# Kernel tuning notes

Hardware: AMD Instinct MI355X
Metric: run time of the kernel (lower is better)

Reference implementation:

```python
import jax, jax.numpy as jnp
import numpy as np
import math

B, S, KV_DIM, Q_DIM, E, H = 16, 8192, 512, 512, 512, 8
D = E // H  # head_dim = 64


def setup_inputs() -> dict:
    key = jax.random.key(0)
    ks = jax.random.split(key, 12)
    s_q = 1.0 / math.sqrt(Q_DIM)
    s_kv = 1.0 / math.sqrt(KV_DIM)
    s_e = 1.0 / math.sqrt(E)
    return {
        "query": jax.random.normal(ks[0], (B, Q_DIM), dtype=jnp.float32),
        "key_value": jax.random.normal(ks[1], (B, S, KV_DIM), dtype=jnp.float32),
        "Wq": jax.random.uniform(ks[2], (Q_DIM, E), jnp.float32, -s_q, s_q),
        "bq": jax.random.uniform(ks[3], (E,), jnp.float32, -s_q, s_q),
        "Wk": jax.random.uniform(ks[4], (KV_DIM, E), jnp.float32, -s_kv, s_kv),
        "bk": jax.random.uniform(ks[5], (E,), jnp.float32, -s_kv, s_kv),
        "Wv": jax.random.uniform(ks[6], (KV_DIM, E), jnp.float32, -s_kv, s_kv),
        "bv": jax.random.uniform(ks[7], (E,), jnp.float32, -s_kv, s_kv),
        "Wo": jax.random.uniform(ks[8], (E, E), jnp.float32, -s_e, s_e),
        "bo": jax.random.uniform(ks[9], (E,), jnp.float32, -s_e, s_e),
    }


def reference(query, key_value, Wq, bq, Wk, bk, Wv, bv, Wo, bo):
    bsz, seq_len, _ = key_value.shape
    # q: [B, H, D] (single query per batch)
    q = (query @ Wq + bq).reshape(bsz, H, D)
    # k, v: [B, S, H, D]
    k = (key_value @ Wk + bk).reshape(bsz, seq_len, H, D)
    v = (key_value @ Wv + bv).reshape(bsz, seq_len, H, D)
    scale = 1.0 / math.sqrt(D)
    # attn logits: [B, H, S]
    attn = jnp.einsum("bhd,bshd->bhs", q, k) * scale
    weights = jax.nn.softmax(attn, axis=-1)
    # context: [B, H, D] -> [B, E]
    context = jnp.einsum("bhs,bshd->bhd", weights, v).reshape(bsz, E)
    return context @ Wo + bo
```

## Files before the change

kernel.cpp:

```cpp
#include <hip/hip_runtime.h>
#include <math.h>

#define B_   16
#define S_   8192
#define KVD  512
#define E_   512
#define H_   8
#define D_   64

#define OFF_QKVEC   0
#define OFF_QBUF    65536
#define OFF_LACC    73728
#define OFF_CTXACC  73856
#define OFF_CTXBUF  139392
#define WS_FLOATS   147584
#define ZERO_START  OFF_QBUF
#define ZERO_COUNT  82048

__global__ __launch_bounds__(256) void k_init(float* __restrict__ wsf,
                                              float* __restrict__ out) {
    int i = blockIdx.x * 256 + threadIdx.x;
    const int nws4 = ZERO_COUNT / 4;
    if (i < nws4) {
        *(float4*)&wsf[ZERO_START + i * 4] = make_float4(0.f, 0.f, 0.f, 0.f);
    } else if (i < nws4 + (B_ * E_) / 4) {
        *(float4*)&out[(i - nws4) * 4] = make_float4(0.f, 0.f, 0.f, 0.f);
    }
}

__global__ __launch_bounds__(512) void k_q(const float* __restrict__ query,
                                           const float* __restrict__ Wq,
                                           float* __restrict__ q_buf) {
    const int kc = blockIdx.x, b = blockIdx.y;
    const int e = threadIdx.x;
    __shared__ float qs[128];
    if (e < 128) qs[e] = query[(size_t)b * 512 + kc * 128 + e];
    __syncthreads();
    const float* wq = Wq + (size_t)(kc * 128) * E_ + e;
    float a0 = 0.f, a1 = 0.f, a2 = 0.f, a3 = 0.f;
    for (int k = 0; k < 128; k += 4) {
        a0 = fmaf(qs[k],     wq[(size_t)(k)     * E_], a0);
        a1 = fmaf(qs[k + 1], wq[(size_t)(k + 1) * E_], a1);
        a2 = fmaf(qs[k + 2], wq[(size_t)(k + 2) * E_], a2);
        a3 = fmaf(qs[k + 3], wq[(size_t)(k + 3) * E_], a3);
    }
    atomicAdd(&q_buf[(size_t)b * E_ + e], (a0 + a1) + (a2 + a3));
}

__global__ __launch_bounds__(256) void k_fold(const float* __restrict__ q_buf,
                                              const float* __restrict__ bq,
                                              const float* __restrict__ Wk,
                                              float* __restrict__ qk_vec) {
    const int cc = blockIdx.x, h = blockIdx.y;
    const int tid = threadIdx.x;
    const int c0 = cc * 64;
    __shared__ float wk[64 * 65];
    __shared__ float qh[16 * 64];

    #pragma unroll
    for (int k = 0; k < 4; ++k) {
        int f4i = tid + k * 256;
        int row = f4i >> 4, d4 = f4i & 15;
        float4 v = *(const float4*)&Wk[(size_t)(c0 + row) * E_ + h * D_ + d4 * 4];
        wk[row * 65 + d4 * 4 + 0] = v.x;
        wk[row * 65 + d4 * 4 + 1] = v.y;
        wk[row * 65 + d4 * 4 + 2] = v.z;
        wk[row * 65 + d4 * 4 + 3] = v.w;
    }
    #pragma unroll
    for (int k = 0; k < 4; ++k) {
        int idx = tid + k * 256;
        int b = idx >> 6, d = idx & 63;
        qh[idx] = (q_buf[(size_t)b * E_ + h * D_ + d] + bq[h * D_ + d]) * 0.125f;
    }
    __syncthreads();

    const int c_local = tid & 63, w = tid >> 6;
    float acc[4] = {0.f, 0.f, 0.f, 0.f};
    for (int d = 0; d < 64; ++d) {
        float wv = wk[c_local * 65 + d];
        #pragma unroll
        for (int i = 0; i < 4; ++i)
            acc[i] = fmaf(qh[(w * 4 + i) * 64 + d], wv, acc[i]);
    }
    #pragma unroll
    for (int i = 0; i < 4; ++i) {
        int b = w * 4 + i;
        qk_vec[((size_t)b * H_ + h) * KVD + c0 + c_local] = acc[i];
    }
}

#define SROW 68
#define RB   4

template <int NC>
__device__ __forceinline__ void attn_loadrows(float (&kvr)[RB][8],
                                              const float* __restrict__ base,
                                              int it, int lane) {
    #pragma unroll
    for (int r = 0; r < RB; ++r) {
        const float* rowp = base + (size_t)(it * RB + r) * KVD;
        float4 v0 = *(const float4*)&rowp[lane * 4];
        float4 v1 = *(const float4*)&rowp[256 + lane * 4];
        kvr[r][0] = v0.x; kvr[r][1] = v0.y; kvr[r][2] = v0.z; kvr[r][3] = v0.w;
        kvr[r][4] = v1.x; kvr[r][5] = v1.y; kvr[r][6] = v1.z; kvr[r][7] = v1.w;
    }
}

__device__ __forceinline__ void attn_process(const float (&kvr)[RB][8],
                                             const float (&qk)[H_][8],
                                             float (&ctx)[H_][8], float& l_run,
                                             float* __restrict__ wscr,
                                             const float* __restrict__ rdb,
                                             int lane) {
    const int seg = lane & 7;
    #pragma unroll
    for (int r = 0; r < RB; ++r)
        #pragma unroll
        for (int h = 0; h < H_; ++h) {
            float p = 0.f;
            #pragma unroll
            for (int j = 0; j < 8; ++j) p = fmaf(kvr[r][j], qk[h][j], p);
            wscr[(r * H_ + h) * SROW + lane] = p;
        }
    float e4[RB];
    #pragma unroll
    for (int r = 0; r < RB; ++r) {
        const float* p = rdb + r * H_ * SROW;
        float4 x = *(const float4*)p;
        float4 y = *(const float4*)(p + 4);
        float s = ((x.x + x.y) + (x.z + x.w)) + ((y.x + y.y) + (y.z + y.w));
        s += __shfl_xor(s, 1);
        s += __shfl_xor(s, 2);
        s += __shfl_xor(s, 4);
        e4[r] = __expf(s);
        l_run += e4[r];
    }
    #pragma unroll
    for (int r = 0; r < RB; ++r)
        #pragma unroll
        for (int h = 0; h < H_; ++h) {
            float wv = __shfl(e4[r], h * 8 + seg);
            #pragma unroll
            for (int j = 0; j < 8; ++j)
                ctx[h][j] = fmaf(wv, kvr[r][j], ctx[h][j]);
        }
}

template <int NC>
__global__ __launch_bounds__(256, 2) void k_attn(const float* __restrict__ kv,
                                                 const float* __restrict__ qk_vec,
                                                 float* __restrict__ ctx_acc,
                                                 float* __restrict__ l_acc) {
    constexpr int CHUNK = S_ / NC;
    constexpr int RPW = CHUNK / 4;
    constexpr int NIT = RPW / RB;
    constexpr int SPW = RB * H_ * SROW;

    __shared__ __align__(16) float scr[4 * SPW];
    __shared__ float lbuf[32];

    const int tid = threadIdx.x;
    const int lane = tid & 63;
    const int w = tid >> 6;
    const int nc = blockIdx.x, b = blockIdx.y;
    const int hme = lane >> 3, seg = lane & 7;

    float qk[H_][8];
    {
        const float* qb = qk_vec + (size_t)b * H_ * KVD;
        #pragma unroll
        for (int h = 0; h < H_; ++h) {
            float4 v0 = *(const float4*)&qb[h * KVD + lane * 4];
            float4 v1 = *(const float4*)&qb[h * KVD + 256 + lane * 4];
            qk[h][0] = v0.x; qk[h][1] = v0.y; qk[h][2] = v0.z; qk[h][3] = v0.w;
            qk[h][4] = v1.x; qk[h][5] = v1.y; qk[h][6] = v1.z; qk[h][7] = v1.w;
        }
    }

    float ctx[H_][8];
    #pragma unroll
    for (int h = 0; h < H_; ++h)
        #pragma unroll
        for (int j = 0; j < 8; ++j) ctx[h][j] = 0.f;
    float l_run = 0.f;

    float* wscr = scr + w * SPW;
    const float* rdb = wscr + hme * SROW + seg * 8;
    const float* kvbase = kv + ((size_t)b * S_ + (size_t)nc * CHUNK + (size_t)w * RPW) * KVD;

    float kvA[RB][8], kvB[RB][8];
    attn_loadrows<NC>(kvA, kvbase, 0, lane);
    #pragma unroll 1
    for (int it = 0; it < NIT; it += 2) {
        attn_loadrows<NC>(kvB, kvbase, it + 1, lane);
        attn_process(kvA, qk, ctx, l_run, wscr, rdb, lane);
        if (it + 2 < NIT) attn_loadrows<NC>(kvA, kvbase, it + 2, lane);
        attn_process(kvB, qk, ctx, l_run, wscr, rdb, lane);
    }

    if (seg == 0) lbuf[w * 8 + hme] = l_run;
    __syncthreads();
    float* cbuf = scr;
    if (w == 0) {
        #pragma unroll
        for (int h = 0; h < H_; ++h) {
            *(float4*)&cbuf[h * KVD + lane * 4] =
                make_float4(ctx[h][0], ctx[h][1], ctx[h][2], ctx[h][3]);
            *(float4*)&cbuf[h * KVD + 256 + lane * 4] =
                make_float4(ctx[h][4], ctx[h][5], ctx[h][6], ctx[h][7]);
        }
    }
    __syncthreads();
    if (w != 0) {
        #pragma unroll
        for (int h = 0; h < H_; ++h) {
            #pragma unroll
            for (int j = 0; j < 4; ++j)
                atomicAdd(&cbuf[h * KVD + lane * 4 + j], ctx[h][j]);
            #pragma unroll
            for (int j = 4; j < 8; ++j)
                atomicAdd(&cbuf[h * KVD + 256 + lane * 4 + (j - 4)], ctx[h][j]);
        }
    }
    __syncthreads();
    size_t gbase = (size_t)b * (H_ * KVD);
    #pragma unroll
    for (int k = 0; k < 16; ++k)
        atomicAdd(&ctx_acc[gbase + k * 256 + tid], cbuf[k * 256 + tid]);
    if (tid < H_) {
        float L = lbuf[tid] + lbuf[8 + tid] + lbuf[16 + tid] + lbuf[24 + tid];
        atomicAdd(&l_acc[b * H_ + tid], L);
    }
}

__global__ __launch_bounds__(512) void k_ctx(const float* __restrict__ ctx_acc,
                                             const float* __restrict__ l_acc,
                                             const float* __restrict__ Wv,
                                             const float* __restrict__ bv,
                                             float* __restrict__ ctx_buf) {
    const int kc = blockIdx.x, b = blockIdx.y;
    const int e = threadIdx.x;
    const int h = e >> 6;
    const float inv = 1.0f / l_acc[b * H_ + h];
    const float* ca = ctx_acc + ((size_t)b * H_ + h) * KVD + kc * 128;
    const float* wv = Wv + (size_t)(kc * 128) * E_ + e;
    float a0 = 0.f, a1 = 0.f, a2 = 0.f, a3 = 0.f;
    for (int c = 0; c < 128; c += 4) {
        a0 = fmaf(ca[c],     wv[(size_t)(c)     * E_], a0);
        a1 = fmaf(ca[c + 1], wv[(size_t)(c + 1) * E_], a1);
        a2 = fmaf(ca[c + 2], wv[(size_t)(c + 2) * E_], a2);
        a3 = fmaf(ca[c + 3], wv[(size_t)(c + 3) * E_], a3);
    }
    float val = ((a0 + a1) + (a2 + a3)) * inv;
    if (kc == 0) val += bv[e];
    atomicAdd(&ctx_buf[(size_t)b * E_ + e], val);
}

__global__ __launch_bounds__(512) void k_o(const float* __restrict__ ctx_buf,
                                           const float* __restrict__ Wo,
                                           const float* __restrict__ bo,
                                           float* __restrict__ out) {
    const int kc = blockIdx.x, b = blockIdx.y;
    const int e = threadIdx.x;
    const float* cs = ctx_buf + (size_t)b * E_ + kc * 128;
    const float* wo = Wo + (size_t)(kc * 128) * E_ + e;
    float a0 = 0.f, a1 = 0.f, a2 = 0.f, a3 = 0.f;
    for (int k = 0; k < 128; k += 4) {
        a0 = fmaf(cs[k],     wo[(size_t)(k)     * E_], a0);
        a1 = fmaf(cs[k + 1], wo[(size_t)(k + 1) * E_], a1);
        a2 = fmaf(cs[k + 2], wo[(size_t)(k + 2) * E_], a2);
        a3 = fmaf(cs[k + 3], wo[(size_t)(k + 3) * E_], a3);
    }
    float val = (a0 + a1) + (a2 + a3);
    if (kc == 0) val += bo[e];
    atomicAdd(&out[(size_t)b * E_ + e], val);
}

extern "C" void kernel_launch(void* const* d_in, const int* in_sizes, int n_in,
                              void* d_out, int out_size, void* d_ws, size_t ws_size,
                              hipStream_t stream) {
    const float* query = (const float*)d_in[0];
    const float* kv    = (const float*)d_in[1];
    const float* Wq    = (const float*)d_in[2];
    const float* bq    = (const float*)d_in[3];
    const float* Wk    = (const float*)d_in[4];
    const float* Wv    = (const float*)d_in[6];
    const float* bv    = (const float*)d_in[7];
    const float* Wo    = (const float*)d_in[8];
    const float* bo    = (const float*)d_in[9];
    float* out = (float*)d_out;
    float* wsf = (float*)d_ws;

    float* qk_vec  = wsf + OFF_QKVEC;
    float* q_buf   = wsf + OFF_QBUF;
    float* l_acc   = wsf + OFF_LACC;
    float* ctx_acc = wsf + OFF_CTXACC;
    float* ctx_buf = wsf + OFF_CTXBUF;

    constexpr int NC = 32;

    k_init<<<89, 256, 0, stream>>>(wsf, out);
    k_q<<<dim3(4, B_), 512, 0, stream>>>(query, Wq, q_buf);
    k_fold<<<dim3(8, H_), 256, 0, stream>>>(q_buf, bq, Wk, qk_vec);
    k_attn<NC><<<dim3(NC, B_), 256, 0, stream>>>(kv, qk_vec, ctx_acc, l_acc);
    k_ctx<<<dim3(4, B_), 512, 0, stream>>>(ctx_acc, l_acc, Wv, bv, ctx_buf);
    k_o<<<dim3(4, B_), 512, 0, stream>>>(ctx_buf, Wo, bo, out);
}
```

Measured before the change: 488.2 us.

## Fuse init, Q projection and K-fold into one prep kernel; relax attn launch bounds

Merges the zero-init, query projection and Wk fold kernels into a single k_prep launch. Each fold block now recomputes its head slice of the Q projection from the full query held in shared memory, which removes the q_buf atomics and two launches but adds redundant Wq reads across the 8 column blocks per head. It also changes k_attn launch bounds from 2 to 1 blocks per CU. That lets the compiler use more registers but may reduce occupancy.

Measured after the change: 454.4 us. 6.9% less time.

```diff
diff --git a/kernel.cpp b/kernel.cpp
--- a/kernel.cpp
+++ b/kernel.cpp
@@ -9,91 +9,96 @@
 #define D_   64
 
 #define OFF_QKVEC   0
-#define OFF_QBUF    65536
-#define OFF_LACC    73728
-#define OFF_CTXACC  73856
-#define OFF_CTXBUF  139392
-#define WS_FLOATS   147584
-#define ZERO_START  OFF_QBUF
-#define ZERO_COUNT  82048
-
-__global__ __launch_bounds__(256) void k_init(float* __restrict__ wsf,
-                                              float* __restrict__ out) {
-    int i = blockIdx.x * 256 + threadIdx.x;
-    const int nws4 = ZERO_COUNT / 4;
-    if (i < nws4) {
-        *(float4*)&wsf[ZERO_START + i * 4] = make_float4(0.f, 0.f, 0.f, 0.f);
-    } else if (i < nws4 + (B_ * E_) / 4) {
-        *(float4*)&out[(i - nws4) * 4] = make_float4(0.f, 0.f, 0.f, 0.f);
-    }
-}
-
-__global__ __launch_bounds__(512) void k_q(const float* __restrict__ query,
-                                           const float* __restrict__ Wq,
-                                           float* __restrict__ q_buf) {
-    const int kc = blockIdx.x, b = blockIdx.y;
-    const int e = threadIdx.x;
-    __shared__ float qs[128];
-    if (e < 128) qs[e] = query[(size_t)b * 512 + kc * 128 + e];
-    __syncthreads();
-    const float* wq = Wq + (size_t)(kc * 128) * E_ + e;
-    float a0 = 0.f, a1 = 0.f, a2 = 0.f, a3 = 0.f;
-    for (int k = 0; k < 128; k += 4) {
-        a0 = fmaf(qs[k],     wq[(size_t)(k)     * E_], a0);
-        a1 = fmaf(qs[k + 1], wq[(size_t)(k + 1) * E_], a1);
-        a2 = fmaf(qs[k + 2], wq[(size_t)(k + 2) * E_], a2);
-        a3 = fmaf(qs[k + 3], wq[(size_t)(k + 3) * E_], a3);
-    }
-    atomicAdd(&q_buf[(size_t)b * E_ + e], (a0 + a1) + (a2 + a3));
-}
-
-__global__ __launch_bounds__(256) void k_fold(const float* __restrict__ q_buf,
+#define OFF_LACC    65536
+#define OFF_CTXACC  65664
+#define OFF_CTXBUF  131200
+#define ZERO_START  OFF_LACC
+#define ZERO_COUNT  73856
+
+__global__ __launch_bounds__(256) void k_prep(const float* __restrict__ query,
+                                              const float* __restrict__ Wq,
                                               const float* __restrict__ bq,
                                               const float* __restrict__ Wk,
-                                              float* __restrict__ qk_vec) {
-    const int cc = blockIdx.x, h = blockIdx.y;
+                                              float* __restrict__ wsf,
+                                              float* __restrict__ out) {
+    const int blk = blockIdx.x;
     const int tid = threadIdx.x;
-    const int c0 = cc * 64;
+
+    if (blk >= 64) {
+        int i = (blk - 64) * 256 + tid;
+        const int nws4 = ZERO_COUNT / 4;
+        if (i < nws4) {
+            *(float4*)&wsf[ZERO_START + i * 4] = make_float4(0.f, 0.f, 0.f, 0.f);
+        } else if (i < nws4 + (B_ * E_) / 4) {
+            *(float4*)&out[(size_t)(i - nws4) * 4] = make_float4(0.f, 0.f, 0.f, 0.f);
+        }
+        return;
+    }
+
+    const int cc = blk & 7, h = blk >> 3;
+    float* qk_vec = wsf + OFF_QKVEC;
+
+    __shared__ float qbuf[16 * 512];
     __shared__ float wk[64 * 65];
     __shared__ float qh[16 * 64];
 
+    #pragma unroll
+    for (int k = 0; k < 8; ++k) {
+        int f4i = tid + k * 256;
+        *(float4*)&qbuf[f4i * 4] = *(const float4*)&query[(size_t)f4i * 4];
+    }
     #pragma unroll
     for (int k = 0; k < 4; ++k) {
         int f4i = tid + k * 256;
         int row = f4i >> 4, d4 = f4i & 15;
-        float4 v = *(const float4*)&Wk[(size_t)(c0 + row) * E_ + h * D_ + d4 * 4];
+        float4 v = *(const float4*)&Wk[(size_t)(cc * 64 + row) * E_ + h * D_ + d4 * 4];
         wk[row * 65 + d4 * 4 + 0] = v.x;
         wk[row * 65 + d4 * 4 + 1] = v.y;
         wk[row * 65 + d4 * 4 + 2] = v.z;
         wk[row * 65 + d4 * 4 + 3] = v.w;
     }
-    #pragma unroll
-    for (int k = 0; k < 4; ++k) {
-        int idx = tid + k * 256;
-        int b = idx >> 6, d = idx & 63;
-        qh[idx] = (q_buf[(size_t)b * E_ + h * D_ + d] + bq[h * D_ + d]) * 0.125f;
-    }
-    __syncthreads();
-
-    const int c_local = tid & 63, w = tid >> 6;
-    float acc[4] = {0.f, 0.f, 0.f, 0.f};
-    for (int d = 0; d < 64; ++d) {
-        float wv = wk[c_local * 65 + d];
+    __syncthreads();
+
+    const int d = tid & 63, w = tid >> 6;
+    {
+        float acc[4] = {0.f, 0.f, 0.f, 0.f};
+        const float* wq = Wq + h * D_ + d;
+        for (int k = 0; k < 512; k += 4) {
+            #pragma unroll
+            for (int kk = 0; kk < 4; ++kk) {
+                float wv = wq[(size_t)(k + kk) * E_];
+                #pragma unroll
+                for (int i = 0; i < 4; ++i)
+                    acc[i] = fmaf(qbuf[(w * 4 + i) * 512 + k + kk], wv, acc[i]);
+            }
+        }
+        float bqv = bq[h * D_ + d];
         #pragma unroll
         for (int i = 0; i < 4; ++i)
-            acc[i] = fmaf(qh[(w * 4 + i) * 64 + d], wv, acc[i]);
-    }
-    #pragma unroll
-    for (int i = 0; i < 4; ++i) {
-        int b = w * 4 + i;
-        qk_vec[((size_t)b * H_ + h) * KVD + c0 + c_local] = acc[i];
+            qh[(w * 4 + i) * 64 + d] = (acc[i] + bqv) * 0.125f;
+    }
+    __syncthreads();
+
+    {
+        const int c_local = tid & 63;
+        float acc[4] = {0.f, 0.f, 0.f, 0.f};
+        for (int dd = 0; dd < 64; ++dd) {
+            float wv = wk[c_local * 65 + dd];
+            #pragma unroll
+            for (int i = 0; i < 4; ++i)
+                acc[i] = fmaf(qh[(w * 4 + i) * 64 + dd], wv, acc[i]);
+        }
+        #pragma unroll
+        for (int i = 0; i < 4; ++i) {
+            int b = w * 4 + i;
+            qk_vec[((size_t)b * H_ + h) * KVD + cc * 64 + c_local] = acc[i];
+        }
     }
 }
 
 #define SROW 68
 #define RB   4
 
-template <int NC>
 __device__ __forceinline__ void attn_loadrows(float (&kvr)[RB][8],
                                               const float* __restrict__ base,
                                               int it, int lane) {
@@ -148,7 +153,7 @@
 }
 
 template <int NC>
-__global__ __launch_bounds__(256, 2) void k_attn(const float* __restrict__ kv,
+__global__ __launch_bounds__(256, 1) void k_attn(const float* __restrict__ kv,
                                                  const float* __restrict__ qk_vec,
                                                  float* __restrict__ ctx_acc,
                                                  float* __restrict__ l_acc) {
@@ -190,12 +195,12 @@
     const float* kvbase = kv + ((size_t)b * S_ + (size_t)nc * CHUNK + (size_t)w * RPW) * KVD;
 
     float kvA[RB][8], kvB[RB][8];
-    attn_loadrows<NC>(kvA, kvbase, 0, lane);
+    attn_loadrows(kvA, kvbase, 0, lane);
     #pragma unroll 1
     for (int it = 0; it < NIT; it += 2) {
-        attn_loadrows<NC>(kvB, kvbase, it + 1, lane);
+        attn_loadrows(kvB, kvbase, it + 1, lane);
         attn_process(kvA, qk, ctx, l_run, wscr, rdb, lane);
-        if (it + 2 < NIT) attn_loadrows<NC>(kvA, kvbase, it + 2, lane);
+        if (it + 2 < NIT) attn_loadrows(kvA, kvbase, it + 2, lane);
         attn_process(kvB, qk, ctx, l_run, wscr, rdb, lane);
     }
 
@@ -293,16 +298,13 @@
     float* wsf = (float*)d_ws;
 
     float* qk_vec  = wsf + OFF_QKVEC;
-    float* q_buf   = wsf + OFF_QBUF;
     float* l_acc   = wsf + OFF_LACC;
     float* ctx_acc = wsf + OFF_CTXACC;
     float* ctx_buf = wsf + OFF_CTXBUF;
 
     constexpr int NC = 32;
 
-    k_init<<<89, 256, 0, stream>>>(wsf, out);
-    k_q<<<dim3(4, B_), 512, 0, stream>>>(query, Wq, q_buf);
-    k_fold<<<dim3(8, H_), 256, 0, stream>>>(q_buf, bq, Wk, qk_vec);
+    k_prep<<<145, 256, 0, stream>>>(query, Wq, bq, Wk, wsf, out);
     k_attn<NC><<<dim3(NC, B_), 256, 0, stream>>>(kv, qk_vec, ctx_acc, l_acc);
     k_ctx<<<dim3(4, B_), 512, 0, stream>>>(ctx_acc, l_acc, Wv, bv, ctx_buf);
     k_o<<<dim3(4, B_), 512, 0, stream>>>(ctx_buf, Wo, bo, out);
```
